# Performance work log

Measured on AMD Instinct MI355X. Metric: run time of the kernel, lower is better.

Reference implementation:

```python
import jax, jax.numpy as jnp
import numpy as np

NUM_ITERATIONS = 3
EPS = 1e-7

def squash(v, axis=-1):
    # scale = |v|^2/(1+|v|^2) * v/sqrt(|v|^2+eps), matching the torch module
    sq = jnp.sum(v * v, axis=axis, keepdims=True)
    return (sq / (1.0 + sq)) * v / jnp.sqrt(sq + EPS)

def setup_inputs() -> dict:
    key = jax.random.key(0)
    kx, kw = jax.random.split(key)
    B, R, C, O, I = 256, 1152, 10, 16, 8
    x = jax.random.normal(kx, (B, R, I), dtype=jnp.float32)
    W = jax.random.normal(kw, (R, C, O, I), dtype=jnp.float32)
    return {"x": x, "W": W}

def reference(x, W):
    B, R, I = x.shape
    C, O = W.shape[1], W.shape[2]
    # u_hat[b,r,c,o] = sum_i W[r,c,o,i] * x[b,r,i]  (batched tiny GEMV)
    u_hat = jnp.einsum('rcoi,bri->brco', W, x)
    b_ij = jnp.zeros((B, R, C), dtype=u_hat.dtype)
    v = None
    for it in range(NUM_ITERATIONS):
        c_ij = jax.nn.softmax(b_ij, axis=1)          # softmax over route nodes (dim=1, as in source)
        s_j = jnp.einsum('brc,brco->bco', c_ij, u_hat)
        v = squash(s_j, axis=-1)                      # squash over out_channels (dim=-2 of the 5D torch tensor)
        if it != NUM_ITERATIONS - 1:
            b_ij = b_ij + jnp.einsum('brco,bco->brc', u_hat, v)
    # match torch output shape (B, 1, C, O, 1)
    return v[:, None, :, :, None]
```

## Files before the change

kernel.cpp:

```cpp
#include <hip/hip_runtime.h>
#include <cstdint>

#define BB 256
#define RR 1152
#define CC 10
#define OO 16
#define II 8
#define NT 768
#define GG 2
#define NWAVE (NT / 64)
#define WPG (NWAVE / GG)
#define LOG2E 1.4426950408889634f
#define WSWORDS ((size_t)RR * CC * (OO * II / 2))

typedef float float2v __attribute__((ext_vector_type(2)));

__device__ __forceinline__ void unpack2(uint32_t pk, float& lo, float& hi) {
    union { uint32_t i; float f; } a, b;
    a.i = pk << 16; b.i = pk & 0xffff0000u;
    lo = a.f; hi = b.f;
}
__device__ __forceinline__ float qpadd1(float v) {
    int o = __builtin_amdgcn_mov_dpp(__float_as_int(v), 0xB1, 0xF, 0xF, true);
    return v + __int_as_float(o);
}
__device__ __forceinline__ float qpadd2(float v) {
    int o = __builtin_amdgcn_mov_dpp(__float_as_int(v), 0x4E, 0xF, 0xF, true);
    return v + __int_as_float(o);
}
__device__ __forceinline__ uint32_t cvtpk(float lo, float hi) {
    uint32_t r;
    asm("v_cvt_pk_bf16_f32 %0, %1, %2" : "=v"(r) : "v"(lo), "v"(hi));
    return r;
}
#if __has_builtin(__builtin_amdgcn_exp2f)
#define EXP2(x) __builtin_amdgcn_exp2f(x)
#else
#define EXP2(x) __expf((x) * 0.6931471805599453f)
#endif
#define LD4(P) (*reinterpret_cast<const float4*>(P))

#define DOT8(PA0, PA1, PA2, PA3, X0, X1, X2, X3, OUT)                         \
  do {                                                                        \
    float2v acc_ = PA0 * X0;                                                  \
    acc_ = __builtin_elementwise_fma(PA1, X1, acc_);                          \
    acc_ = __builtin_elementwise_fma(PA2, X2, acc_);                          \
    acc_ = __builtin_elementwise_fma(PA3, X3, acc_);                          \
    OUT = acc_.x + acc_.y;                                                    \
  } while (0)

#define UNPK(WQ, P0, P1, P2, P3)                                              \
  do {                                                                        \
    float lo_, hi_;                                                           \
    unpack2(WQ.x, lo_, hi_); P0 = (float2v){lo_, hi_};                        \
    unpack2(WQ.y, lo_, hi_); P1 = (float2v){lo_, hi_};                        \
    unpack2(WQ.z, lo_, hi_); P2 = (float2v){lo_, hi_};                        \
    unpack2(WQ.w, lo_, hi_); P3 = (float2v){lo_, hi_};                        \
  } while (0)

__global__ __launch_bounds__(256)
void k_cvt(const float* __restrict__ Wf, uint32_t* __restrict__ wbf) {
    size_t i = ((size_t)blockIdx.x * 256 + threadIdx.x) * 4;
    if (i < WSWORDS) {
        float4 a = LD4(Wf + 2 * i);
        float4 b = LD4(Wf + 2 * i + 4);
        uint4 r;
        r.x = cvtpk(a.x, a.y); r.y = cvtpk(a.z, a.w);
        r.z = cvtpk(b.x, b.y); r.w = cvtpk(b.z, b.w);
        *reinterpret_cast<uint4*>(wbf + i) = r;
    }
}

__global__ __launch_bounds__(NT, 6)
void k_caps(const float* __restrict__ x, const uint32_t* __restrict__ wb,
            float* __restrict__ out) {
    extern __shared__ uint32_t u2[];
    __shared__ float p0s[NWAVE][8][2][GG];
    __shared__ float part2[2][17][NWAVE];

    const int t = threadIdx.x;
    const int c  = blockIdx.x / (BB / GG);
    const int b0 = (blockIdx.x % (BB / GG)) * GG;
    const int wv = t >> 6, l = t & 63;
    const int rg = t >> 3, p = t & 7;

    uint32_t* uA = u2;
    uint32_t* uB = u2 + (size_t)RR * 8;
    uint32_t* wrA = uA + (size_t)rg * 8 + p;
    uint32_t* wrB = uB + (size_t)rg * 8 + p;

    float s00 = 0.f, s01 = 0.f, s10 = 0.f, s11 = 0.f;
#pragma unroll 2
    for (int it = 0; it < 12; ++it) {
        const int r = it * 96 + rg;
        const uint32_t* wrow = wb + ((size_t)r * CC + c) * 64 + 4 * p;
        uint4 wq0 = *reinterpret_cast<const uint4*>(wrow);
        uint4 wq1 = *reinterpret_cast<const uint4*>(wrow + 32);
        const float* xp = x + ((size_t)b0 * RR + r) * II;
        float4 xa0 = LD4(xp);
        float4 xa1 = LD4(xp + 4);
        float4 xg0 = LD4(xp + (size_t)RR * II);
        float4 xg1 = LD4(xp + (size_t)RR * II + 4);
        float2v A0, A1, A2, A3, B0, B1, B2, B3;
        UNPK(wq0, A0, A1, A2, A3);
        UNPK(wq1, B0, B1, B2, B3);
        float2v X0 = { xa0.x, xa0.y }, X1 = { xa0.z, xa0.w };
        float2v X2 = { xa1.x, xa1.y }, X3 = { xa1.z, xa1.w };
        float2v Y0 = { xg0.x, xg0.y }, Y1 = { xg0.z, xg0.w };
        float2v Y2 = { xg1.x, xg1.y }, Y3 = { xg1.z, xg1.w };
        float d0, d1, e0, e1;
        DOT8(A0, A1, A2, A3, X0, X1, X2, X3, d0);
        DOT8(B0, B1, B2, B3, X0, X1, X2, X3, d1);
        DOT8(A0, A1, A2, A3, Y0, Y1, Y2, Y3, e0);
        DOT8(B0, B1, B2, B3, Y0, Y1, Y2, Y3, e1);
        s00 += d0; s01 += d1; s10 += e0; s11 += e1;
        wrA[(size_t)it * 768] = cvtpk(d0, d1);
        wrB[(size_t)it * 768] = cvtpk(e0, e1);
    }
#pragma unroll
    for (int m = 8; m < 64; m <<= 1) {
        s00 += __shfl_xor(s00, m); s01 += __shfl_xor(s01, m);
        s10 += __shfl_xor(s10, m); s11 += __shfl_xor(s11, m);
    }
    if (l < 8) {
        p0s[wv][l][0][0] = s00; p0s[wv][l][1][0] = s01;
        p0s[wv][l][0][1] = s10; p0s[wv][l][1][1] = s11;
    }
    __syncthreads();

    const int g2 = wv / WPG;
    const int wv6 = wv - g2 * WPG;
    const uint32_t* ug = g2 ? uB : uA;
    const int q = l & 3;
    const int rl = l >> 2;
    const int rbase = wv6 * 16 + rl;
    const uint32_t* rp = ug + (size_t)rbase * 8 + 2 * q;

    const int oo = l & 15;
    const int gb = l & 48;
    const int t0 = gb | (2 * q), t1 = gb | (2 * q + 1);
    const int t2 = gb | (2 * q + 8), t3 = gb | (2 * q + 9);

    float ra, rb, rc, rd;
    {
        float sv = 0.f;
#pragma unroll
        for (int w = 0; w < NWAVE; ++w) sv += p0s[w][oo & 7][oo >> 3][g2];
        sv *= (1.0f / RR);
        float ss = sv * sv;
        ss += __shfl_xor(ss, 1); ss += __shfl_xor(ss, 2);
        ss += __shfl_xor(ss, 4); ss += __shfl_xor(ss, 8);
        float vv = sv * (ss / ((1.0f + ss) * sqrtf(ss + 1e-7f)));
        ra = __shfl(vv, t0); rb = __shfl(vv, t1);
        rc = __shfl(vv, t2); rd = __shfl(vv, t3);
    }

#pragma unroll
    for (int pass = 1; pass < 3; ++pass) {
        const float2v WQA = { ra * LOG2E, rc * LOG2E };
        const float2v WQB = { rb * LOG2E, rd * LOG2E };
        float2v N0 = { 0.f, 0.f }, N1 = { 0.f, 0.f };
        float den = 0.f;

#pragma unroll
        for (int it2 = 0; it2 < 12; ++it2) {
            uint2 pp = *reinterpret_cast<const uint2*>(rp + (size_t)it2 * 768);
            float a_, b_, c_, d_;
            unpack2(pp.x, a_, b_);
            unpack2(pp.y, c_, d_);
            float2v P0 = { a_, b_ };
            float2v P1 = { c_, d_ };
            float2v lg2 = __builtin_elementwise_fma(P0, WQA, P1 * WQB);
            float lg = lg2.x + lg2.y;
            lg = qpadd1(lg);
            lg = qpadd2(lg);
            float e = EXP2(lg);
            den += e;
            float2v E2 = { e, e };
            N0 = __builtin_elementwise_fma(E2, P0, N0);
            N1 = __builtin_elementwise_fma(E2, P1, N1);
        }

        float n0 = N0.x, n2 = N0.y, n1 = N1.x, n3 = N1.y;
#pragma unroll
        for (int m = 4; m < 64; m <<= 1) {
            n0 += __shfl_xor(n0, m); n1 += __shfl_xor(n1, m);
            n2 += __shfl_xor(n2, m); n3 += __shfl_xor(n3, m);
            den += __shfl_xor(den, m);
        }
        const int pb = pass & 1;
        if (l < 4) {
            part2[pb][2 * l][wv]     = n0;
            part2[pb][2 * l + 1][wv] = n1;
            part2[pb][2 * l + 8][wv] = n2;
            part2[pb][2 * l + 9][wv] = n3;
            if (l == 0) part2[pb][16][wv] = den;
        }
        __syncthreads();

        const float* po = &part2[pb][oo][0];
        const float* pd = &part2[pb][16][0];
        float nf = 0.f, df = 0.f;
#pragma unroll
        for (int w = 0; w < WPG; ++w) {
            nf += po[g2 * WPG + w];
            df += pd[g2 * WPG + w];
        }
        float s2 = nf / df;
        float ss2 = s2 * s2;
        ss2 += __shfl_xor(ss2, 1); ss2 += __shfl_xor(ss2, 2);
        ss2 += __shfl_xor(ss2, 4); ss2 += __shfl_xor(ss2, 8);
        float vv2 = s2 * (ss2 / ((1.0f + ss2) * sqrtf(ss2 + 1e-7f)));

        if (pass == 1) {
            ra += __shfl(vv2, t0); rb += __shfl(vv2, t1);
            rc += __shfl(vv2, t2); rd += __shfl(vv2, t3);
        } else {
            if ((wv == 0 || wv == WPG) && l < 16)
                out[((size_t)(b0 + g2) * CC + c) * OO + oo] = vv2;
        }
    }
}

extern "C" void kernel_launch(void* const* d_in, const int* in_sizes, int n_in,
                              void* d_out, int out_size, void* d_ws, size_t ws_size,
                              hipStream_t stream) {
    const float* x = (const float*)d_in[0];
    const float* W = (const float*)d_in[1];
    if (n_in >= 2 && in_sizes[0] == RR * CC * OO * II &&
        in_sizes[1] == BB * RR * II) {
        const float* tmp = x; x = W; W = tmp;
    }
    float* out = (float*)d_out;
    uint32_t* wbf = (uint32_t*)d_ws;

    const int cvt_blocks = (int)((WSWORDS / 4 + 255) / 256);
    k_cvt<<<cvt_blocks, 256, 0, stream>>>(W, wbf);

    const size_t dyn_lds = (size_t)GG * RR * 8 * 4;
    k_caps<<<CC * (BB / GG), NT, dyn_lds, stream>>>(x, wbf, out);
}
```

Before: 110.2 us.

## Pack x to bf16 and compute u_hat with v_dot2_f32_bf16

```diff
diff --git a/kernel.cpp b/kernel.cpp
--- a/kernel.cpp
+++ b/kernel.cpp
@@ -12,6 +12,7 @@
 #define WPG (NWAVE / GG)
 #define LOG2E 1.4426950408889634f
 #define WSWORDS ((size_t)RR * CC * (OO * II / 2))
+#define XWORDS  ((size_t)BB * RR * (II / 2))
 
 typedef float float2v __attribute__((ext_vector_type(2)));
 
@@ -32,6 +33,11 @@
     uint32_t r;
     asm("v_cvt_pk_bf16_f32 %0, %1, %2" : "=v"(r) : "v"(lo), "v"(hi));
     return r;
+}
+__device__ __forceinline__ float dot2bf(uint32_t a, uint32_t b, float c) {
+    float d;
+    asm("v_dot2_f32_bf16 %0, %1, %2, %3" : "=v"(d) : "v"(a), "v"(b), "v"(c));
+    return d;
 }
 #if __has_builtin(__builtin_amdgcn_exp2f)
 #define EXP2(x) __builtin_amdgcn_exp2f(x)
@@ -40,39 +46,38 @@
 #endif
 #define LD4(P) (*reinterpret_cast<const float4*>(P))
 
-#define DOT8(PA0, PA1, PA2, PA3, X0, X1, X2, X3, OUT)                         \
+#define DOT8P(WQ, XQ, OUT)                                                    \
   do {                                                                        \
-    float2v acc_ = PA0 * X0;                                                  \
-    acc_ = __builtin_elementwise_fma(PA1, X1, acc_);                          \
-    acc_ = __builtin_elementwise_fma(PA2, X2, acc_);                          \
-    acc_ = __builtin_elementwise_fma(PA3, X3, acc_);                          \
-    OUT = acc_.x + acc_.y;                                                    \
+    float a_ = dot2bf(WQ.x, XQ.x, 0.0f);                                      \
+    a_ = dot2bf(WQ.y, XQ.y, a_);                                              \
+    a_ = dot2bf(WQ.z, XQ.z, a_);                                              \
+    OUT = dot2bf(WQ.w, XQ.w, a_);                                             \
   } while (0)
 
-#define UNPK(WQ, P0, P1, P2, P3)                                              \
-  do {                                                                        \
-    float lo_, hi_;                                                           \
-    unpack2(WQ.x, lo_, hi_); P0 = (float2v){lo_, hi_};                        \
-    unpack2(WQ.y, lo_, hi_); P1 = (float2v){lo_, hi_};                        \
-    unpack2(WQ.z, lo_, hi_); P2 = (float2v){lo_, hi_};                        \
-    unpack2(WQ.w, lo_, hi_); P3 = (float2v){lo_, hi_};                        \
-  } while (0)
-
 __global__ __launch_bounds__(256)
-void k_cvt(const float* __restrict__ Wf, uint32_t* __restrict__ wbf) {
-    size_t i = ((size_t)blockIdx.x * 256 + threadIdx.x) * 4;
-    if (i < WSWORDS) {
-        float4 a = LD4(Wf + 2 * i);
-        float4 b = LD4(Wf + 2 * i + 4);
+void k_cvt(const float* __restrict__ Wf, const float* __restrict__ xf,
+           uint32_t* __restrict__ wbf, uint32_t* __restrict__ xpk) {
+    size_t tid = (size_t)blockIdx.x * 256 + threadIdx.x;
+    if (tid < WSWORDS / 4) {
+        float4 a = LD4(Wf + 8 * tid);
+        float4 b = LD4(Wf + 8 * tid + 4);
         uint4 r;
         r.x = cvtpk(a.x, a.y); r.y = cvtpk(a.z, a.w);
         r.z = cvtpk(b.x, b.y); r.w = cvtpk(b.z, b.w);
-        *reinterpret_cast<uint4*>(wbf + i) = r;
+        *reinterpret_cast<uint4*>(wbf + 4 * tid) = r;
+    }
+    if (tid < XWORDS / 4) {
+        float4 a = LD4(xf + 8 * tid);
+        float4 b = LD4(xf + 8 * tid + 4);
+        uint4 r;
+        r.x = cvtpk(a.x, a.y); r.y = cvtpk(a.z, a.w);
+        r.z = cvtpk(b.x, b.y); r.w = cvtpk(b.z, b.w);
+        *reinterpret_cast<uint4*>(xpk + 4 * tid) = r;
     }
 }
 
 __global__ __launch_bounds__(NT, 6)
-void k_caps(const float* __restrict__ x, const uint32_t* __restrict__ wb,
+void k_caps(const uint32_t* __restrict__ xpk, const uint32_t* __restrict__ wb,
             float* __restrict__ out) {
     extern __shared__ uint32_t u2[];
     __shared__ float p0s[NWAVE][8][2][GG];
@@ -90,29 +95,20 @@
     uint32_t* wrB = uB + (size_t)rg * 8 + p;
 
     float s00 = 0.f, s01 = 0.f, s10 = 0.f, s11 = 0.f;
-#pragma unroll 2
+#pragma unroll 4
     for (int it = 0; it < 12; ++it) {
         const int r = it * 96 + rg;
         const uint32_t* wrow = wb + ((size_t)r * CC + c) * 64 + 4 * p;
         uint4 wq0 = *reinterpret_cast<const uint4*>(wrow);
         uint4 wq1 = *reinterpret_cast<const uint4*>(wrow + 32);
-        const float* xp = x + ((size_t)b0 * RR + r) * II;
-        float4 xa0 = LD4(xp);
-        float4 xa1 = LD4(xp + 4);
-        float4 xg0 = LD4(xp + (size_t)RR * II);
-        float4 xg1 = LD4(xp + (size_t)RR * II + 4);
-        float2v A0, A1, A2, A3, B0, B1, B2, B3;
-        UNPK(wq0, A0, A1, A2, A3);
-        UNPK(wq1, B0, B1, B2, B3);
-        float2v X0 = { xa0.x, xa0.y }, X1 = { xa0.z, xa0.w };
-        float2v X2 = { xa1.x, xa1.y }, X3 = { xa1.z, xa1.w };
-        float2v Y0 = { xg0.x, xg0.y }, Y1 = { xg0.z, xg0.w };
-        float2v Y2 = { xg1.x, xg1.y }, Y3 = { xg1.z, xg1.w };
+        const uint32_t* xp = xpk + ((size_t)b0 * RR + r) * 4;
+        uint4 xq0 = *reinterpret_cast<const uint4*>(xp);
+        uint4 xq1 = *reinterpret_cast<const uint4*>(xp + (size_t)RR * 4);
         float d0, d1, e0, e1;
-        DOT8(A0, A1, A2, A3, X0, X1, X2, X3, d0);
-        DOT8(B0, B1, B2, B3, X0, X1, X2, X3, d1);
-        DOT8(A0, A1, A2, A3, Y0, Y1, Y2, Y3, e0);
-        DOT8(B0, B1, B2, B3, Y0, Y1, Y2, Y3, e1);
+        DOT8P(wq0, xq0, d0);
+        DOT8P(wq1, xq0, d1);
+        DOT8P(wq0, xq1, e0);
+        DOT8P(wq1, xq1, e1);
         s00 += d0; s01 += d1; s10 += e0; s11 += e1;
         wrA[(size_t)it * 768] = cvtpk(d0, d1);
         wrB[(size_t)it * 768] = cvtpk(e0, e1);
@@ -233,10 +229,11 @@
     }
     float* out = (float*)d_out;
     uint32_t* wbf = (uint32_t*)d_ws;
-
-    const int cvt_blocks = (int)((WSWORDS / 4 + 255) / 256);
-    k_cvt<<<cvt_blocks, 256, 0, stream>>>(W, wbf);
+    uint32_t* xpk = wbf + WSWORDS;
+
+    const int cvt_blocks = (int)((XWORDS / 4 + 255) / 256);
+    k_cvt<<<cvt_blocks, 256, 0, stream>>>(W, x, wbf, xpk);
 
     const size_t dyn_lds = (size_t)GG * RR * 8 * 4;
-    k_caps<<<CC * (BB / GG), NT, dyn_lds, stream>>>(x, wbf, out);
-}
+    k_caps<<<CC * (BB / GG), NT, dyn_lds, stream>>>(xpk, wbf, out);
+}
```

After: 101.9 us. 1.08x faster.
